# Kernel optimization log

Hardware: AMD Instinct MI355X
Metric: run time of the kernel (lower is better)

Reference implementation:

```python
import jax, jax.numpy as jnp
import numpy as np

N_HOPS = 3
EDGE_RATE = 0.5   # quirk: floor(rate+u)==1 KEEPS an edge with prob=rate, scaled by 1/(1-rate)
MESS_RATE = 0.1   # standard dropout: zero with prob p, scale kept by 1/(1-p)
N_USERS = 50000
N_ITEMS = 100000
N_NODES = N_USERS + N_ITEMS
NNZ = 1000000
D = 64


def setup_inputs() -> dict:
    key = jax.random.key(0)
    k_u, k_i, k_r, k_c, k_v = jax.random.split(key, 5)
    return {
        "user_embed": jax.random.normal(k_u, (N_USERS, D), dtype=jnp.float32),
        "item_embed": jax.random.normal(k_i, (N_ITEMS, D), dtype=jnp.float32),
        "rows": jax.random.randint(k_r, (NNZ,), 0, N_NODES),
        "cols": jax.random.randint(k_c, (NNZ,), 0, N_NODES),
        "vals": jax.random.uniform(k_v, (NNZ,), dtype=jnp.float32),
    }


def reference(user_embed, item_embed, rows, cols, vals):
    n_users = user_embed.shape[0]
    n_nodes = n_users + item_embed.shape[0]

    all_embed = jnp.concatenate([user_embed, item_embed], axis=0)  # [N, D]
    agg = all_embed
    embs = [all_embed]

    key = jax.random.key(42)
    for hop in range(N_HOPS):
        key, k_e, k_m = jax.random.split(key, 3)
        # edge dropout (faithful to torch._sparse_dropout): keep iff floor(rate+u)==1
        u = jax.random.uniform(k_e, (vals.shape[0],), dtype=vals.dtype)
        keep = (EDGE_RATE + u) >= 1.0
        v = jnp.where(keep, vals, jnp.zeros_like(vals)) * (1.0 / (1.0 - EDGE_RATE))
        # SpMM: out[r] += v * agg[c]  (zeroed edges contribute nothing, same math as
        # rebuilding a smaller sparse tensor, without dynamic shapes)
        msgs = v[:, None] * agg[cols]                       # [nnz, D]
        agg = jax.ops.segment_sum(msgs, rows, num_segments=n_nodes)
        # message dropout (nn.Dropout): zero with prob p, scale kept by 1/(1-p)
        m = jax.random.bernoulli(k_m, 1.0 - MESS_RATE, agg.shape)
        agg = jnp.where(m, agg / (1.0 - MESS_RATE), jnp.zeros_like(agg))
        embs.append(agg)

    embs = jnp.stack(embs, axis=1)  # [N, n_hops+1, D]
    return embs[:n_users], embs[n_users:]
```

## Files before the change

### kernel.cpp

```cpp
#include <hip/hip_runtime.h>
#include <stdint.h>


static constexpr int kUsers = 50000;
static constexpr int kItems = 100000;
static constexpr int kNodes = kUsers + kItems;
static constexpr int kNnz   = 1000000;
static constexpr int kD     = 64;
static constexpr int kHops  = 3;
static constexpr int kRowF  = (kHops + 1) * kD;

static constexpr int kScanBlocks = 147;
static constexpr int kCntN       = kScanBlocks * 1024;

__host__ __device__ inline void tf2x32(uint32_t k0, uint32_t k1,
                                       uint32_t x0, uint32_t x1,
                                       uint32_t &o0, uint32_t &o1) {
  uint32_t ks2 = k0 ^ k1 ^ 0x1BD11BDAu;
  x0 += k0; x1 += k1;
#define TF_R(r) { x0 += x1; x1 = (x1 << (r)) | (x1 >> (32 - (r))); x1 ^= x0; }
  TF_R(13) TF_R(15) TF_R(26) TF_R(6)   x0 += k1;  x1 += ks2 + 1u;
  TF_R(17) TF_R(29) TF_R(16) TF_R(24)  x0 += ks2; x1 += k0 + 2u;
  TF_R(13) TF_R(15) TF_R(26) TF_R(6)   x0 += k0;  x1 += k1 + 3u;
  TF_R(17) TF_R(29) TF_R(16) TF_R(24)  x0 += k1;  x1 += ks2 + 4u;
  TF_R(13) TF_R(15) TF_R(26) TF_R(6)   x0 += ks2; x1 += k0 + 5u;
#undef TF_R
  o0 = x0; o1 = x1;
}

__device__ inline uint32_t jax_bits32(uint32_t k0, uint32_t k1, uint32_t i) {
  uint32_t b1, b2;
  tf2x32(k0, k1, 0u, i, b1, b2);
  return b1 ^ b2;
}

__device__ inline float bits_to_unit(uint32_t b) {
  return __uint_as_float((b >> 9) | 0x3f800000u) - 1.0f;
}


__global__ __launch_bounds__(256) void init_slice0(
    const float4* __restrict__ user, const float4* __restrict__ item,
    float4* __restrict__ out) {
  int i = blockIdx.x * 256 + threadIdx.x;
  if (i >= kNodes * 16) return;
  int node = i >> 4, q = i & 15;
  float4 v = (node < kUsers) ? user[node * 16 + q]
                             : item[(node - kUsers) * 16 + q];
  out[(size_t)node * (kRowF / 4) + q] = v;
}

__global__ __launch_bounds__(256) void hist_kernel(
    const int* __restrict__ rows, int* __restrict__ cnt) {
  int e = blockIdx.x * 256 + threadIdx.x;
  if (e >= kNnz) return;
  atomicAdd(&cnt[rows[e]], 1);
}

__global__ __launch_bounds__(256) void scanA(
    const int* __restrict__ cnt, int* __restrict__ partials) {
  int t = threadIdx.x;
  int4 v = ((const int4*)(cnt + blockIdx.x * 1024))[t];
  int s = v.x + v.y + v.z + v.w;
  __shared__ int sh[256];
  sh[t] = s; __syncthreads();
  for (int off = 128; off > 0; off >>= 1) {
    if (t < off) sh[t] += sh[t + off];
    __syncthreads();
  }
  if (t == 0) partials[blockIdx.x] = sh[0];
}

__global__ __launch_bounds__(256) void scanB(int* __restrict__ partials) {
  int t = threadIdx.x;
  int v = (t < kScanBlocks) ? partials[t] : 0;
  __shared__ int sh[256];
  sh[t] = v; __syncthreads();
  for (int off = 1; off < 256; off <<= 1) {
    int a = (t >= off) ? sh[t - off] : 0;
    __syncthreads();
    sh[t] += a;
    __syncthreads();
  }
  if (t < kScanBlocks) partials[t] = sh[t] - v;
}

__global__ __launch_bounds__(256) void scanC(
    const int* __restrict__ cnt, const int* __restrict__ partials,
    int* __restrict__ X) {
  int t = threadIdx.x;
  int4 v = ((const int4*)(cnt + blockIdx.x * 1024))[t];
  int s = v.x + v.y + v.z + v.w;
  __shared__ int sh[256];
  sh[t] = s; __syncthreads();
  for (int off = 1; off < 256; off <<= 1) {
    int a = (t >= off) ? sh[t - off] : 0;
    __syncthreads();
    sh[t] += a;
    __syncthreads();
  }
  int base = partials[blockIdx.x] + sh[t] - s;
  int4 o;
  o.x = base; o.y = base + v.x; o.z = o.y + v.y; o.w = o.z + v.z;
  ((int4*)(X + blockIdx.x * 1024))[t] = o;
}

__global__ __launch_bounds__(256) void scatter_kernel(
    const int* __restrict__ rows, const int* __restrict__ cols,
    const float* __restrict__ vals, int* __restrict__ X,
    int* __restrict__ cols_s, float* __restrict__ v2,
    uint32_t e00, uint32_t e01, uint32_t e10, uint32_t e11,
    uint32_t e20, uint32_t e21) {
  int e = blockIdx.x * 256 + threadIdx.x;
  if (e >= kNnz) return;
  int r = rows[e];
  int pos = atomicAdd(&X[r], 1);
  cols_s[pos] = cols[e];
  float v = vals[e] * 2.0f;
  float u0 = bits_to_unit(jax_bits32(e00, e01, (uint32_t)e));
  float u1 = bits_to_unit(jax_bits32(e10, e11, (uint32_t)e));
  float u2 = bits_to_unit(jax_bits32(e20, e21, (uint32_t)e));
  v2[pos]            = (0.5f + u0 >= 1.0f) ? v : 0.0f;
  v2[kNnz + pos]     = (0.5f + u1 >= 1.0f) ? v : 0.0f;
  v2[2 * kNnz + pos] = (0.5f + u2 >= 1.0f) ? v : 0.0f;
}

__global__ __launch_bounds__(256) void csr_spmm(
    const int* __restrict__ X, const int* __restrict__ cols_s,
    const float* __restrict__ v2h, float* __restrict__ out, int hop,
    uint32_t km0, uint32_t km1) {
  int wid = blockIdx.x * 4 + (threadIdx.x >> 6);
  if (wid >= kNodes) return;
  int lane = threadIdx.x & 63;
  int g = lane >> 4, q = lane & 15;
  int s = (wid == 0) ? 0 : X[wid - 1];
  int t = X[wid];
  float4 acc = make_float4(0.f, 0.f, 0.f, 0.f);
  const float* src = out + (size_t)hop * kD;
  for (int i = s + g; i < t; i += 4) {
    float v = v2h[i];
    if (v != 0.0f) {
      int c = cols_s[i];
      float4 x = *(const float4*)(src + (size_t)c * kRowF + (q << 2));
      acc.x += v * x.x; acc.y += v * x.y; acc.z += v * x.z; acc.w += v * x.w;
    }
  }
  acc.x += __shfl_xor(acc.x, 16); acc.y += __shfl_xor(acc.y, 16);
  acc.z += __shfl_xor(acc.z, 16); acc.w += __shfl_xor(acc.w, 16);
  acc.x += __shfl_xor(acc.x, 32); acc.y += __shfl_xor(acc.y, 32);
  acc.z += __shfl_xor(acc.z, 32); acc.w += __shfl_xor(acc.w, 32);
  float u = bits_to_unit(jax_bits32(km0, km1, (uint32_t)(wid * kD + lane)));
  float m = (u < 0.9f) ? (1.0f / 0.9f) : 0.0f;
  float m0 = __shfl(m, (q << 2) + 0);
  float m1 = __shfl(m, (q << 2) + 1);
  float m2 = __shfl(m, (q << 2) + 2);
  float m3 = __shfl(m, (q << 2) + 3);
  if (g == 0) {
    float4 r = make_float4(acc.x * m0, acc.y * m1, acc.z * m2, acc.w * m3);
    *(float4*)(out + (size_t)wid * kRowF + (hop + 1) * kD + (q << 2)) = r;
  }
}

__global__ __launch_bounds__(256) void init_full(
    const float4* __restrict__ user, const float4* __restrict__ item,
    float4* __restrict__ out) {
  int i = blockIdx.x * 256 + threadIdx.x;
  if (i >= kNodes * 16) return;
  int node = i >> 4, q = i & 15;
  float4 v = (node < kUsers) ? user[node * 16 + q]
                             : item[(node - kUsers) * 16 + q];
  float4 z = make_float4(0.f, 0.f, 0.f, 0.f);
  float4* row = out + (size_t)node * (kRowF / 4);
  row[q] = v; row[16 + q] = z; row[32 + q] = z; row[48 + q] = z;
}

__global__ __launch_bounds__(256) void spmm_atomic(
    const int* __restrict__ rows, const int* __restrict__ cols,
    const float* __restrict__ vals, float* __restrict__ out, int hop,
    uint32_t k0, uint32_t k1) {
  int e = (int)((blockIdx.x * 256u + threadIdx.x) >> 6);
  if (e >= kNnz) return;
  int lane = threadIdx.x & 63;
  float u = bits_to_unit(jax_bits32(k0, k1, (uint32_t)e));
  if (!(0.5f + u >= 1.0f)) return;
  float v = vals[e] * 2.0f;
  int r = rows[e], c = cols[e];
  float msg = v * out[(size_t)c * kRowF + hop * kD + lane];
  atomicAdd(&out[(size_t)r * kRowF + (hop + 1) * kD + lane], msg);
}

__global__ __launch_bounds__(256) void mdrop_kernel(
    float* __restrict__ out, int hop, uint32_t k0, uint32_t k1) {
  const int total = kNodes * kD;
  int j = blockIdx.x * 256 + threadIdx.x;
  if (j >= total) return;
  float u = bits_to_unit(jax_bits32(k0, k1, (uint32_t)j));
  int node = j >> 6, d = j & 63;
  size_t idx = (size_t)node * kRowF + (hop + 1) * kD + d;
  float a = out[idx];
  out[idx] = (u < 0.9f) ? a / 0.9f : 0.0f;
}

extern "C" void kernel_launch(void* const* d_in, const int* in_sizes, int n_in,
                              void* d_out, int out_size, void* d_ws, size_t ws_size,
                              hipStream_t stream) {
  const float* user = (const float*)d_in[0];
  const float* item = (const float*)d_in[1];
  const int*   rows = (const int*)d_in[2];
  const int*   cols = (const int*)d_in[3];
  const float* vals = (const float*)d_in[4];
  float* out = (float*)d_out;

  uint32_t k0 = 0u, k1 = 42u;
  uint32_t ke[kHops][2], km[kHops][2];
  for (int hop = 0; hop < kHops; ++hop) {
    uint32_t n0, n1;
    tf2x32(k0, k1, 0u, 0u, n0, n1);
    tf2x32(k0, k1, 0u, 1u, ke[hop][0], ke[hop][1]);
    tf2x32(k0, k1, 0u, 2u, km[hop][0], km[hop][1]);
    k0 = n0; k1 = n1;
  }

  const size_t cnt_b  = (size_t)kCntN * 4;
  const size_t x_b    = (size_t)kCntN * 4;
  const size_t cols_b = (size_t)kNnz * 4;
  const size_t v2_b   = (size_t)kHops * kNnz * 4;
  const size_t par_b  = 1024;
  const size_t need   = cnt_b + x_b + cols_b + v2_b + par_b;

  if (ws_size >= need) {
    char* ws = (char*)d_ws;
    int*   cnt      = (int*)ws;
    int*   X        = (int*)(ws + cnt_b);
    int*   cols_s   = (int*)(ws + cnt_b + x_b);
    float* v2       = (float*)(ws + cnt_b + x_b + cols_b);
    int*   partials = (int*)(ws + cnt_b + x_b + cols_b + v2_b);

    init_slice0<<<(kNodes * 16 + 255) / 256, 256, 0, stream>>>(
        (const float4*)user, (const float4*)item, (float4*)out);

    hipMemsetAsync(cnt, 0, cnt_b, stream);
    hist_kernel<<<(kNnz + 255) / 256, 256, 0, stream>>>(rows, cnt);
    scanA<<<kScanBlocks, 256, 0, stream>>>(cnt, partials);
    scanB<<<1, 256, 0, stream>>>(partials);
    scanC<<<kScanBlocks, 256, 0, stream>>>(cnt, partials, X);
    scatter_kernel<<<(kNnz + 255) / 256, 256, 0, stream>>>(
        rows, cols, vals, X, cols_s, v2,
        ke[0][0], ke[0][1], ke[1][0], ke[1][1], ke[2][0], ke[2][1]);

    for (int hop = 0; hop < kHops; ++hop) {
      csr_spmm<<<kNodes / 4, 256, 0, stream>>>(
          X, cols_s, v2 + (size_t)hop * kNnz, out, hop,
          km[hop][0], km[hop][1]);
    }
  } else {
    init_full<<<(kNodes * 16 + 255) / 256, 256, 0, stream>>>(
        (const float4*)user, (const float4*)item, (float4*)out);
    for (int hop = 0; hop < kHops; ++hop) {
      spmm_atomic<<<(kNnz * 64 + 255) / 256, 256, 0, stream>>>(
          rows, cols, vals, out, hop, ke[hop][0], ke[hop][1]);
      mdrop_kernel<<<(kNodes * kD + 255) / 256, 256, 0, stream>>>(
          out, hop, km[hop][0], km[hop][1]);
    }
  }
}
```

Baseline: 326.7 us.

## Pack edge column, per-hop keep bits and value into one 8-byte record

The scatter kernel now writes one uint2 per edge: the column index with three per-hop edge-dropout keep bits in its top bits, plus the scaled value. This replaces a separate column array and three per-hop value arrays. The SpMM reads that single record and tests the hop's bit. It also switches to 8 edge groups of 8 lanes, each lane loading two float4s, to raise edge-level parallelism per wavefront. This cuts scatter write traffic and gives one coalesced load per edge, but each hop now reads 8 bytes per edge where it read 4 for a dropped edge, and the shuffle reduction gains a level.

```diff
diff --git a/kernel.cpp b/kernel.cpp
--- a/kernel.cpp
+++ b/kernel.cpp
@@ -108,56 +108,66 @@
 __global__ __launch_bounds__(256) void scatter_kernel(
     const int* __restrict__ rows, const int* __restrict__ cols,
     const float* __restrict__ vals, int* __restrict__ X,
-    int* __restrict__ cols_s, float* __restrict__ v2,
+    uint2* __restrict__ ed,
     uint32_t e00, uint32_t e01, uint32_t e10, uint32_t e11,
     uint32_t e20, uint32_t e21) {
   int e = blockIdx.x * 256 + threadIdx.x;
   if (e >= kNnz) return;
   int r = rows[e];
   int pos = atomicAdd(&X[r], 1);
-  cols_s[pos] = cols[e];
-  float v = vals[e] * 2.0f;
   float u0 = bits_to_unit(jax_bits32(e00, e01, (uint32_t)e));
   float u1 = bits_to_unit(jax_bits32(e10, e11, (uint32_t)e));
   float u2 = bits_to_unit(jax_bits32(e20, e21, (uint32_t)e));
-  v2[pos]            = (0.5f + u0 >= 1.0f) ? v : 0.0f;
-  v2[kNnz + pos]     = (0.5f + u1 >= 1.0f) ? v : 0.0f;
-  v2[2 * kNnz + pos] = (0.5f + u2 >= 1.0f) ? v : 0.0f;
+  uint32_t packed = (uint32_t)cols[e]
+                  | ((0.5f + u0 >= 1.0f) ? (1u << 29) : 0u)
+                  | ((0.5f + u1 >= 1.0f) ? (1u << 30) : 0u)
+                  | ((0.5f + u2 >= 1.0f) ? (1u << 31) : 0u);
+  ed[pos] = make_uint2(packed, __float_as_uint(vals[e] * 2.0f));
 }
 
 __global__ __launch_bounds__(256) void csr_spmm(
-    const int* __restrict__ X, const int* __restrict__ cols_s,
-    const float* __restrict__ v2h, float* __restrict__ out, int hop,
-    uint32_t km0, uint32_t km1) {
+    const int* __restrict__ X, const uint2* __restrict__ ed,
+    float* __restrict__ out, int hop, uint32_t km0, uint32_t km1) {
   int wid = blockIdx.x * 4 + (threadIdx.x >> 6);
   if (wid >= kNodes) return;
   int lane = threadIdx.x & 63;
-  int g = lane >> 4, q = lane & 15;
+  int g = lane >> 3, q = lane & 7;
   int s = (wid == 0) ? 0 : X[wid - 1];
   int t = X[wid];
-  float4 acc = make_float4(0.f, 0.f, 0.f, 0.f);
+  float4 a0 = make_float4(0.f, 0.f, 0.f, 0.f);
+  float4 a1 = make_float4(0.f, 0.f, 0.f, 0.f);
   const float* src = out + (size_t)hop * kD;
-  for (int i = s + g; i < t; i += 4) {
-    float v = v2h[i];
-    if (v != 0.0f) {
-      int c = cols_s[i];
-      float4 x = *(const float4*)(src + (size_t)c * kRowF + (q << 2));
-      acc.x += v * x.x; acc.y += v * x.y; acc.z += v * x.z; acc.w += v * x.w;
+  const uint32_t kbit = 1u << (29 + hop);
+  for (int i = s + g; i < t; i += 8) {
+    uint2 m = ed[i];
+    if (m.x & kbit) {
+      float v = __uint_as_float(m.y);
+      int c = (int)(m.x & 0x3FFFFu);
+      const float* p = src + (size_t)c * kRowF + (q << 3);
+      float4 x0 = *(const float4*)p;
+      float4 x1 = *(const float4*)(p + 4);
+      a0.x += v * x0.x; a0.y += v * x0.y; a0.z += v * x0.z; a0.w += v * x0.w;
+      a1.x += v * x1.x; a1.y += v * x1.y; a1.z += v * x1.z; a1.w += v * x1.w;
     }
   }
-  acc.x += __shfl_xor(acc.x, 16); acc.y += __shfl_xor(acc.y, 16);
-  acc.z += __shfl_xor(acc.z, 16); acc.w += __shfl_xor(acc.w, 16);
-  acc.x += __shfl_xor(acc.x, 32); acc.y += __shfl_xor(acc.y, 32);
-  acc.z += __shfl_xor(acc.z, 32); acc.w += __shfl_xor(acc.w, 32);
+#pragma unroll
+  for (int msk = 8; msk <= 32; msk <<= 1) {
+    a0.x += __shfl_xor(a0.x, msk); a0.y += __shfl_xor(a0.y, msk);
+    a0.z += __shfl_xor(a0.z, msk); a0.w += __shfl_xor(a0.w, msk);
+    a1.x += __shfl_xor(a1.x, msk); a1.y += __shfl_xor(a1.y, msk);
+    a1.z += __shfl_xor(a1.z, msk); a1.w += __shfl_xor(a1.w, msk);
+  }
   float u = bits_to_unit(jax_bits32(km0, km1, (uint32_t)(wid * kD + lane)));
-  float m = (u < 0.9f) ? (1.0f / 0.9f) : 0.0f;
-  float m0 = __shfl(m, (q << 2) + 0);
-  float m1 = __shfl(m, (q << 2) + 1);
-  float m2 = __shfl(m, (q << 2) + 2);
-  float m3 = __shfl(m, (q << 2) + 3);
+  float mk = (u < 0.9f) ? (1.0f / 0.9f) : 0.0f;
+  float mv[8];
+#pragma unroll
+  for (int j = 0; j < 8; ++j) mv[j] = __shfl(mk, (q << 3) + j);
   if (g == 0) {
-    float4 r = make_float4(acc.x * m0, acc.y * m1, acc.z * m2, acc.w * m3);
-    *(float4*)(out + (size_t)wid * kRowF + (hop + 1) * kD + (q << 2)) = r;
+    float4 r0 = make_float4(a0.x * mv[0], a0.y * mv[1], a0.z * mv[2], a0.w * mv[3]);
+    float4 r1 = make_float4(a1.x * mv[4], a1.y * mv[5], a1.z * mv[6], a1.w * mv[7]);
+    float* dst = out + (size_t)wid * kRowF + (hop + 1) * kD + (q << 3);
+    *(float4*)dst = r0;
+    *(float4*)(dst + 4) = r1;
   }
 }
 
@@ -221,20 +231,18 @@
     k0 = n0; k1 = n1;
   }
 
-  const size_t cnt_b  = (size_t)kCntN * 4;
-  const size_t x_b    = (size_t)kCntN * 4;
-  const size_t cols_b = (size_t)kNnz * 4;
-  const size_t v2_b   = (size_t)kHops * kNnz * 4;
-  const size_t par_b  = 1024;
-  const size_t need   = cnt_b + x_b + cols_b + v2_b + par_b;
+  const size_t cnt_b = (size_t)kCntN * 4;
+  const size_t x_b   = (size_t)kCntN * 4;
+  const size_t ed_b  = (size_t)kNnz * 8;
+  const size_t par_b = 1024;
+  const size_t need  = cnt_b + x_b + ed_b + par_b;
 
   if (ws_size >= need) {
     char* ws = (char*)d_ws;
     int*   cnt      = (int*)ws;
     int*   X        = (int*)(ws + cnt_b);
-    int*   cols_s   = (int*)(ws + cnt_b + x_b);
-    float* v2       = (float*)(ws + cnt_b + x_b + cols_b);
-    int*   partials = (int*)(ws + cnt_b + x_b + cols_b + v2_b);
+    uint2* ed       = (uint2*)(ws + cnt_b + x_b);
+    int*   partials = (int*)(ws + cnt_b + x_b + ed_b);
 
     init_slice0<<<(kNodes * 16 + 255) / 256, 256, 0, stream>>>(
         (const float4*)user, (const float4*)item, (float4*)out);
@@ -245,13 +253,12 @@
     scanB<<<1, 256, 0, stream>>>(partials);
     scanC<<<kScanBlocks, 256, 0, stream>>>(cnt, partials, X);
     scatter_kernel<<<(kNnz + 255) / 256, 256, 0, stream>>>(
-        rows, cols, vals, X, cols_s, v2,
+        rows, cols, vals, X, ed,
         ke[0][0], ke[0][1], ke[1][0], ke[1][1], ke[2][0], ke[2][1]);
 
     for (int hop = 0; hop < kHops; ++hop) {
       csr_spmm<<<kNodes / 4, 256, 0, stream>>>(
-          X, cols_s, v2 + (size_t)hop * kNnz, out, hop,
-          km[hop][0], km[hop][1]);
+          X, ed, out, hop, km[hop][0], km[hop][1]);
     }
   } else {
     init_full<<<(kNodes * 16 + 255) / 256, 256, 0, stream>>>(
```

Measured after the change: 301.9 us. 7.6% less time.
